# Kernel optimization log

Measured on AMD Instinct MI355X. Metric: run time of the kernel, lower is better.

The kernel has to match this reference:

```python
import jax, jax.numpy as jnp
import numpy as np

EPS = 1e-12

def setup_inputs() -> dict:
    key = jax.random.key(0)
    k1, k2 = jax.random.split(key)
    B, C, H, W = 16, 256, 64, 64
    x1 = jax.random.normal(k1, (B, C, H, W), dtype=jnp.float32)
    x2 = jax.random.normal(k2, (B, C, H, W), dtype=jnp.float32)
    return {"x1": x1, "x2": x2}

def _l2norm(x):
    # F.normalize(p=2, dim=2, eps=1e-12): divide by max(norm, eps)
    n = jnp.linalg.norm(x, axis=2, keepdims=True)
    return x / jnp.maximum(n, EPS)

def reference(x1, x2):
    B, C, H, W = x1.shape
    x111 = x1.reshape(B, C, H * W)            # [B,C,N]
    x211 = x2.reshape(B, C, H * W)
    x11 = _l2norm(x111)
    x21 = _l2norm(x211)
    # four CxC score matmuls, fused pairwise adds
    attn1 = jnp.einsum('bcn,bdn->bcd', x11, x11)
    attn2 = jnp.einsum('bcn,bdn->bcd', x21, x21)
    attn0 = jnp.einsum('bcn,bdn->bcd', x21, x11)
    attn00 = jnp.einsum('bcn,bdn->bcd', x11, x21)
    attn11 = jax.nn.softmax(attn1 + attn0, axis=-1)   # [B,C,C]
    attn22 = jax.nn.softmax(attn2 + attn00, axis=-1)
    # back-projection, torch transpose(1,2).reshape(B,C,H,W) semantics
    y1 = jnp.einsum('bcd,bdn->bcn', attn11, x111)     # [B,C,N]
    y2 = jnp.einsum('bcd,bdn->bcn', attn22, x211)
    x1_o = jnp.swapaxes(y1, 1, 2).reshape(B, C, H, W) + x1
    x2_o = jnp.swapaxes(y2, 1, 2).reshape(B, C, H, W) + x2
    return x1_o + x2_o
```

## Files before the change

### kernel.cpp

```cpp
#include <hip/hip_runtime.h>
#include <hip/hip_bf16.h>

#define B_ 16
#define C_ 256
#define N_ 4096
#define CN_ (C_ * N_)

typedef __attribute__((ext_vector_type(8))) short bf16x8_t;
typedef __attribute__((ext_vector_type(4))) float f32x4_t;

__device__ __forceinline__ unsigned short f2bf(float f) {
    __hip_bfloat16 h = __float2bfloat16(f);
    return __builtin_bit_cast(unsigned short, h);
}
__device__ __forceinline__ float bf2f(unsigned short u) {
    return __builtin_bit_cast(float, (unsigned int)u << 16);
}

__global__ __launch_bounds__(256) void knorm(const float* __restrict__ x1,
                                             const float* __restrict__ x2,
                                             unsigned short* __restrict__ x1n,
                                             unsigned short* __restrict__ x2n,
                                             float* __restrict__ norms) {
    int row = blockIdx.x;
    int t = threadIdx.x;
    const float4* r1 = (const float4*)(x1 + (size_t)row * N_);
    const float4* r2 = (const float4*)(x2 + (size_t)row * N_);
    float4 a[4], b[4];
    float s1 = 0.f, s2 = 0.f;
#pragma unroll
    for (int p = 0; p < 4; ++p) {
        a[p] = r1[p * 256 + t];
        b[p] = r2[p * 256 + t];
        s1 += a[p].x * a[p].x + a[p].y * a[p].y + a[p].z * a[p].z + a[p].w * a[p].w;
        s2 += b[p].x * b[p].x + b[p].y * b[p].y + b[p].z * b[p].z + b[p].w * b[p].w;
    }
#pragma unroll
    for (int m = 32; m; m >>= 1) { s1 += __shfl_xor(s1, m); s2 += __shfl_xor(s2, m); }
    __shared__ float red[2][4];
    int wid = t >> 6;
    if ((t & 63) == 0) { red[0][wid] = s1; red[1][wid] = s2; }
    __syncthreads();
    s1 = red[0][0] + red[0][1] + red[0][2] + red[0][3];
    s2 = red[1][0] + red[1][1] + red[1][2] + red[1][3];
    float n1 = fmaxf(sqrtf(s1), 1e-12f);
    float n2 = fmaxf(sqrtf(s2), 1e-12f);
    if (t == 0) {
        int bb = row >> 8, cc = row & 255;
        norms[(bb * 2 + 0) * 256 + cc] = n1;
        norms[(bb * 2 + 1) * 256 + cc] = n2;
    }
    float i1 = 1.0f / n1, i2 = 1.0f / n2;
    unsigned short* o1 = x1n + (size_t)row * N_;
    unsigned short* o2 = x2n + (size_t)row * N_;
#pragma unroll
    for (int p = 0; p < 4; ++p) {
        ushort4 w1, w2;
        w1.x = f2bf(a[p].x * i1); w1.y = f2bf(a[p].y * i1);
        w1.z = f2bf(a[p].z * i1); w1.w = f2bf(a[p].w * i1);
        w2.x = f2bf(b[p].x * i2); w2.y = f2bf(b[p].y * i2);
        w2.z = f2bf(b[p].z * i2); w2.w = f2bf(b[p].w * i2);
        *(ushort4*)(o1 + (size_t)(p * 256 + t) * 4) = w1;
        *(ushort4*)(o2 + (size_t)(p * 256 + t) * 4) = w2;
    }
}

__device__ __forceinline__ uint4 bf16x8_add(uint4 a, uint4 b) {
    const unsigned short* pa = (const unsigned short*)&a;
    const unsigned short* pb = (const unsigned short*)&b;
    uint4 res;
    unsigned short* pr = (unsigned short*)&res;
#pragma unroll
    for (int i = 0; i < 8; ++i) pr[i] = f2bf(bf2f(pa[i]) + bf2f(pb[i]));
    return res;
}

__global__ __launch_bounds__(256) void klogits(const unsigned short* __restrict__ x1n,
                                               const unsigned short* __restrict__ x2n,
                                               float* __restrict__ logits) {
    int bid = blockIdx.x;
    int xcd = bid & 7;
    int u = bid >> 3;
    int b = xcd + 8 * (u & 1);
    int tw = u >> 1;
    int w = tw & 1;
    int tile = tw >> 1;
    int c0 = (tile & 3) * 64;
    int d0 = (tile >> 2) * 64;

    const unsigned short* A1 = x1n + (size_t)b * CN_;
    const unsigned short* A2 = x2n + (size_t)b * CN_;
    const unsigned short* Bp = (w ? x2n : x1n) + (size_t)b * CN_;

    __shared__ unsigned short sA[64][72];
    __shared__ unsigned short sB[64][72];

    int t = threadIdx.x, lane = t & 63, wid = t >> 6;
    int wc = wid >> 1, wd = wid & 1;

    f32x4_t acc[2][2];
#pragma unroll
    for (int i = 0; i < 2; ++i)
#pragma unroll
        for (int j = 0; j < 2; ++j) acc[i][j] = 0.f;

    int srow = t >> 3, scol = (t & 7) * 8;

    for (int ks = 0; ks < 64; ++ks) {
        int k0 = ks * 64;
#pragma unroll
        for (int p = 0; p < 2; ++p) {
            int r = srow + p * 32;
            uint4 va = *(const uint4*)(A1 + (size_t)(c0 + r) * N_ + k0 + scol);
            uint4 vb = *(const uint4*)(A2 + (size_t)(c0 + r) * N_ + k0 + scol);
            *(uint4*)&sA[r][scol] = bf16x8_add(va, vb);
            uint4 vB = *(const uint4*)(Bp + (size_t)(d0 + r) * N_ + k0 + scol);
            *(uint4*)&sB[r][scol] = vB;
        }
        __syncthreads();
#pragma unroll
        for (int ksub = 0; ksub < 2; ++ksub) {
            int kc = ksub * 32 + (lane >> 4) * 8;
            bf16x8_t a0 = *(const bf16x8_t*)&sA[wc * 32 + (lane & 15)][kc];
            bf16x8_t a1 = *(const bf16x8_t*)&sA[wc * 32 + 16 + (lane & 15)][kc];
            bf16x8_t b0 = *(const bf16x8_t*)&sB[wd * 32 + (lane & 15)][kc];
            bf16x8_t b1 = *(const bf16x8_t*)&sB[wd * 32 + 16 + (lane & 15)][kc];
            acc[0][0] = __builtin_amdgcn_mfma_f32_16x16x32_bf16(a0, b0, acc[0][0], 0, 0, 0);
            acc[0][1] = __builtin_amdgcn_mfma_f32_16x16x32_bf16(a0, b1, acc[0][1], 0, 0, 0);
            acc[1][0] = __builtin_amdgcn_mfma_f32_16x16x32_bf16(a1, b0, acc[1][0], 0, 0, 0);
            acc[1][1] = __builtin_amdgcn_mfma_f32_16x16x32_bf16(a1, b1, acc[1][1], 0, 0, 0);
        }
        __syncthreads();
    }

    float* outp = logits + ((size_t)((b * 2 + w) * 256 + c0 + wc * 32)) * 256 + d0 + wd * 32;
    int orow = (lane >> 4) * 4, ocol = lane & 15;
#pragma unroll
    for (int mi = 0; mi < 2; ++mi)
#pragma unroll
        for (int ni = 0; ni < 2; ++ni)
#pragma unroll
            for (int r = 0; r < 4; ++r)
                outp[(size_t)(mi * 16 + orow + r) * 256 + ni * 16 + ocol] = acc[mi][ni][r];
}

__global__ __launch_bounds__(64) void ksoftmax(const float* __restrict__ logits,
                                               const float* __restrict__ norms,
                                               unsigned short* __restrict__ attnp) {
    int rid = blockIdx.x;
    int l = threadIdx.x;
    const float* row = logits + (size_t)rid * 256;
    int bw = rid >> 8;
    float v[4];
    float m = -1e30f;
#pragma unroll
    for (int j = 0; j < 4; ++j) { v[j] = row[j * 64 + l]; m = fmaxf(m, v[j]); }
#pragma unroll
    for (int s = 32; s; s >>= 1) m = fmaxf(m, __shfl_xor(m, s));
    float sum = 0.f;
#pragma unroll
    for (int j = 0; j < 4; ++j) { v[j] = __expf(v[j] - m); sum += v[j]; }
#pragma unroll
    for (int s = 32; s; s >>= 1) sum += __shfl_xor(sum, s);
    float rs = 1.0f / sum;
    unsigned short* outp = attnp + (size_t)rid * 256;
    const float* nr = norms + (size_t)bw * 256;
#pragma unroll
    for (int j = 0; j < 4; ++j)
        outp[j * 64 + l] = f2bf(v[j] * rs * nr[j * 64 + l]);
}

__global__ __launch_bounds__(256) void kout(const unsigned short* __restrict__ x1n,
                                            const unsigned short* __restrict__ x2n,
                                            const unsigned short* __restrict__ attnp,
                                            const float* __restrict__ x1,
                                            const float* __restrict__ x2,
                                            float* __restrict__ out) {
    int bid = blockIdx.x;
    int xcd = bid & 7;
    int u = bid >> 3;
    int b = xcd + 8 * (u & 1);
    int rest = u >> 1;
    int n0 = (rest >> 1) * 64;
    int c0 = (rest & 1) * 128;

    __shared__ unsigned short sA1[64][72];
    __shared__ unsigned short sA2[64][72];
    __shared__ unsigned short sB1[128][72];
    __shared__ unsigned short sB2[128][72];

    const unsigned short* A1 = x1n + (size_t)b * CN_;
    const unsigned short* A2 = x2n + (size_t)b * CN_;
    const unsigned short* B1 = attnp + ((size_t)(b * 2 + 0) * 256 + c0) * 256;
    const unsigned short* B2 = attnp + ((size_t)(b * 2 + 1) * 256 + c0) * 256;

    int t = threadIdx.x, lane = t & 63, wc = t >> 6;

    f32x4_t acc1[4][2], acc2[4][2];
#pragma unroll
    for (int i = 0; i < 4; ++i)
#pragma unroll
        for (int j = 0; j < 2; ++j) { acc1[i][j] = 0.f; acc2[i][j] = 0.f; }

    int dl = t >> 3, n8 = (t & 7) * 8;

    for (int ks = 0; ks < 4; ++ks) {
        int k0 = ks * 64;
#pragma unroll
        for (int p = 0; p < 2; ++p) {
            int d = dl + p * 32;
            uint4 va = *(const uint4*)(A1 + (size_t)(k0 + d) * N_ + n0 + n8);
            const unsigned short* pv = (const unsigned short*)&va;
#pragma unroll
            for (int j = 0; j < 8; ++j) sA1[n8 + j][d] = pv[j];
            uint4 vb = *(const uint4*)(A2 + (size_t)(k0 + d) * N_ + n0 + n8);
            const unsigned short* pw = (const unsigned short*)&vb;
#pragma unroll
            for (int j = 0; j < 8; ++j) sA2[n8 + j][d] = pw[j];
        }
#pragma unroll
        for (int p = 0; p < 4; ++p) {
            int cc = dl + p * 32;
            *(uint4*)&sB1[cc][n8] = *(const uint4*)(B1 + (size_t)cc * 256 + k0 + n8);
            *(uint4*)&sB2[cc][n8] = *(const uint4*)(B2 + (size_t)cc * 256 + k0 + n8);
        }
        __syncthreads();
#pragma unroll
        for (int ksub = 0; ksub < 2; ++ksub) {
            int kc = ksub * 32 + (lane >> 4) * 8;
            bf16x8_t a1f[4], a2f[4], b1f[2], b2f[2];
#pragma unroll
            for (int mi = 0; mi < 4; ++mi) {
                a1f[mi] = *(const bf16x8_t*)&sA1[mi * 16 + (lane & 15)][kc];
                a2f[mi] = *(const bf16x8_t*)&sA2[mi * 16 + (lane & 15)][kc];
            }
#pragma unroll
            for (int ci = 0; ci < 2; ++ci) {
                b1f[ci] = *(const bf16x8_t*)&sB1[wc * 32 + ci * 16 + (lane & 15)][kc];
                b2f[ci] = *(const bf16x8_t*)&sB2[wc * 32 + ci * 16 + (lane & 15)][kc];
            }
#pragma unroll
            for (int mi = 0; mi < 4; ++mi)
#pragma unroll
                for (int ci = 0; ci < 2; ++ci) {
                    acc1[mi][ci] = __builtin_amdgcn_mfma_f32_16x16x32_bf16(a1f[mi], b1f[ci], acc1[mi][ci], 0, 0, 0);
                    acc2[mi][ci] = __builtin_amdgcn_mfma_f32_16x16x32_bf16(a2f[mi], b2f[ci], acc2[mi][ci], 0, 0, 0);
                }
        }
        __syncthreads();
    }

    const size_t obase = (size_t)b * CN_;
    int orow = (lane >> 4) * 4, ocol = lane & 15;
#pragma unroll
    for (int mi = 0; mi < 4; ++mi)
#pragma unroll
        for (int ci = 0; ci < 2; ++ci)
#pragma unroll
            for (int r = 0; r < 4; ++r) {
                int n = n0 + mi * 16 + orow + r;
                int c = c0 + wc * 32 + ci * 16 + ocol;
                size_t f = obase + (size_t)n * 256 + c;
                out[f] = acc1[mi][ci][r] + acc2[mi][ci][r] + x1[f] + x2[f];
            }
}

extern "C" void kernel_launch(void* const* d_in, const int* in_sizes, int n_in,
                              void* d_out, int out_size, void* d_ws, size_t ws_size,
                              hipStream_t stream) {
    const float* x1 = (const float*)d_in[0];
    const float* x2 = (const float*)d_in[1];
    float* out = (float*)d_out;

    char* ws = (char*)d_ws;
    unsigned short* x1n  = (unsigned short*)(ws);
    unsigned short* x2n  = (unsigned short*)(ws + 33554432);
    float*          logits = (float*)(ws + 67108864);
    unsigned short* attnp  = (unsigned short*)(ws + 75497472);
    float*          norms  = (float*)(ws + 79691776);

    knorm<<<4096, 256, 0, stream>>>(x1, x2, x1n, x2n, norms);
    klogits<<<512, 256, 0, stream>>>(x1n, x2n, logits);
    ksoftmax<<<8192, 64, 0, stream>>>(logits, norms, attnp);
    kout<<<2048, 256, 0, stream>>>(x1n, x2n, attnp, x1, x2, out);
}
```

Baseline: 297.8 us.

## Precompute normalized sum and bf16 residual, use direct global-to-LDS loads with swizzle

knorm now also writes the sum of the two normalized inputs and a bf16 copy of x1+x2. This removes the per-tile bf16 add in klogits and lets kout read a bf16 residual instead of two fp32 inputs. klogits computes both logit halves in one block that shares the A tile, and stages tiles with global_load_lds into XOR-swizzled LDS. kout loads attention tiles the same way and transposes the A tile into swizzled LDS, and ksoftmax packs four rows per block. The residual rounded to bf16 loses accuracy in the output, and knorm writes more data.

Result: faster. 272.6 us (-8.5%).

```diff
diff --git a/kernel.cpp b/kernel.cpp
--- a/kernel.cpp
+++ b/kernel.cpp
@@ -8,19 +8,29 @@
 
 typedef __attribute__((ext_vector_type(8))) short bf16x8_t;
 typedef __attribute__((ext_vector_type(4))) float f32x4_t;
-
-__device__ __forceinline__ unsigned short f2bf(float f) {
+typedef unsigned int u32;
+typedef unsigned short u16;
+
+__device__ __forceinline__ u16 f2bf(float f) {
     __hip_bfloat16 h = __float2bfloat16(f);
-    return __builtin_bit_cast(unsigned short, h);
-}
-__device__ __forceinline__ float bf2f(unsigned short u) {
-    return __builtin_bit_cast(float, (unsigned int)u << 16);
+    return __builtin_bit_cast(u16, h);
+}
+__device__ __forceinline__ float bf2f(u16 u) {
+    return __builtin_bit_cast(float, (u32)u << 16);
+}
+
+__device__ __forceinline__ void gl_lds16(const void* g, void* l) {
+    __builtin_amdgcn_global_load_lds(
+        (const __attribute__((address_space(1))) u32*)(g),
+        (__attribute__((address_space(3))) u32*)(l), 16, 0, 0);
 }
 
 __global__ __launch_bounds__(256) void knorm(const float* __restrict__ x1,
                                              const float* __restrict__ x2,
-                                             unsigned short* __restrict__ x1n,
-                                             unsigned short* __restrict__ x2n,
+                                             u16* __restrict__ x1n,
+                                             u16* __restrict__ x2n,
+                                             u16* __restrict__ sN,
+                                             u16* __restrict__ sxb,
                                              float* __restrict__ norms) {
     int row = blockIdx.x;
     int t = threadIdx.x;
@@ -51,104 +61,118 @@
         norms[(bb * 2 + 1) * 256 + cc] = n2;
     }
     float i1 = 1.0f / n1, i2 = 1.0f / n2;
-    unsigned short* o1 = x1n + (size_t)row * N_;
-    unsigned short* o2 = x2n + (size_t)row * N_;
+    u16* o1 = x1n + (size_t)row * N_;
+    u16* o2 = x2n + (size_t)row * N_;
+    u16* os = sN + (size_t)row * N_;
+    u16* or_ = sxb + (size_t)row * N_;
 #pragma unroll
     for (int p = 0; p < 4; ++p) {
-        ushort4 w1, w2;
+        ushort4 w1, w2, ws, wr;
         w1.x = f2bf(a[p].x * i1); w1.y = f2bf(a[p].y * i1);
         w1.z = f2bf(a[p].z * i1); w1.w = f2bf(a[p].w * i1);
         w2.x = f2bf(b[p].x * i2); w2.y = f2bf(b[p].y * i2);
         w2.z = f2bf(b[p].z * i2); w2.w = f2bf(b[p].w * i2);
-        *(ushort4*)(o1 + (size_t)(p * 256 + t) * 4) = w1;
-        *(ushort4*)(o2 + (size_t)(p * 256 + t) * 4) = w2;
-    }
-}
-
-__device__ __forceinline__ uint4 bf16x8_add(uint4 a, uint4 b) {
-    const unsigned short* pa = (const unsigned short*)&a;
-    const unsigned short* pb = (const unsigned short*)&b;
-    uint4 res;
-    unsigned short* pr = (unsigned short*)&res;
-#pragma unroll
-    for (int i = 0; i < 8; ++i) pr[i] = f2bf(bf2f(pa[i]) + bf2f(pb[i]));
-    return res;
-}
-
-__global__ __launch_bounds__(256) void klogits(const unsigned short* __restrict__ x1n,
-                                               const unsigned short* __restrict__ x2n,
+        ws.x = f2bf(a[p].x * i1 + b[p].x * i2); ws.y = f2bf(a[p].y * i1 + b[p].y * i2);
+        ws.z = f2bf(a[p].z * i1 + b[p].z * i2); ws.w = f2bf(a[p].w * i1 + b[p].w * i2);
+        wr.x = f2bf(a[p].x + b[p].x); wr.y = f2bf(a[p].y + b[p].y);
+        wr.z = f2bf(a[p].z + b[p].z); wr.w = f2bf(a[p].w + b[p].w);
+        size_t off = (size_t)(p * 256 + t) * 4;
+        *(ushort4*)(o1 + off) = w1;
+        *(ushort4*)(o2 + off) = w2;
+        *(ushort4*)(os + off) = ws;
+        *(ushort4*)(or_ + off) = wr;
+    }
+}
+
+__global__ __launch_bounds__(256) void klogits(const u16* __restrict__ sN,
+                                               const u16* __restrict__ x1n,
+                                               const u16* __restrict__ x2n,
                                                float* __restrict__ logits) {
     int bid = blockIdx.x;
     int xcd = bid & 7;
     int u = bid >> 3;
     int b = xcd + 8 * (u & 1);
-    int tw = u >> 1;
-    int w = tw & 1;
-    int tile = tw >> 1;
+    int tile = u >> 1;
     int c0 = (tile & 3) * 64;
     int d0 = (tile >> 2) * 64;
 
-    const unsigned short* A1 = x1n + (size_t)b * CN_;
-    const unsigned short* A2 = x2n + (size_t)b * CN_;
-    const unsigned short* Bp = (w ? x2n : x1n) + (size_t)b * CN_;
-
-    __shared__ unsigned short sA[64][72];
-    __shared__ unsigned short sB[64][72];
+    __shared__ u16 lds[3 * 4096];
 
     int t = threadIdx.x, lane = t & 63, wid = t >> 6;
-    int wc = wid >> 1, wd = wid & 1;
-
-    f32x4_t acc[2][2];
+    int w = wid & 1, chalf = wid >> 1;
+
+    const char* tb[3];
+    tb[0] = (const char*)(sN  + (size_t)b * CN_ + (size_t)c0 * N_);
+    tb[1] = (const char*)(x1n + (size_t)b * CN_ + (size_t)d0 * N_);
+    tb[2] = (const char*)(x2n + (size_t)b * CN_ + (size_t)d0 * N_);
+    const char* gsrc[6];
+    char* ldst[6];
+#pragma unroll
+    for (int qq = 0; qq < 6; ++qq) {
+        int q = wid * 6 + qq;
+        int ti = q >> 3;
+        int s0 = (q & 7) * 1024 + lane * 16;
+        int rrow = s0 >> 7, inner = s0 & 127;
+        gsrc[qq] = tb[ti] + (size_t)rrow * (N_ * 2) + (inner ^ ((rrow & 7) << 4));
+        ldst[qq] = (char*)lds + q * 1024;
+    }
+
+    f32x4_t acc[2][4];
 #pragma unroll
     for (int i = 0; i < 2; ++i)
 #pragma unroll
-        for (int j = 0; j < 2; ++j) acc[i][j] = 0.f;
-
-    int srow = t >> 3, scol = (t & 7) * 8;
+        for (int j = 0; j < 4; ++j) acc[i][j] = 0.f;
+
+    const char* Abase = (const char*)lds;
+    const char* Bbase = (const char*)(lds + (1 + w) * 4096);
+    int kl = (lane >> 4) * 16;
+    int rA0 = chalf * 32 + (lane & 15);
 
     for (int ks = 0; ks < 64; ++ks) {
-        int k0 = ks * 64;
-#pragma unroll
-        for (int p = 0; p < 2; ++p) {
-            int r = srow + p * 32;
-            uint4 va = *(const uint4*)(A1 + (size_t)(c0 + r) * N_ + k0 + scol);
-            uint4 vb = *(const uint4*)(A2 + (size_t)(c0 + r) * N_ + k0 + scol);
-            *(uint4*)&sA[r][scol] = bf16x8_add(va, vb);
-            uint4 vB = *(const uint4*)(Bp + (size_t)(d0 + r) * N_ + k0 + scol);
-            *(uint4*)&sB[r][scol] = vB;
+        int kbyte = ks * 128;
+#pragma unroll
+        for (int qq = 0; qq < 6; ++qq)
+            gl_lds16(gsrc[qq] + kbyte, ldst[qq]);
+        __syncthreads();
+#pragma unroll
+        for (int ksub = 0; ksub < 2; ++ksub) {
+            int kc = ksub * 64 + kl;
+            bf16x8_t af[2], bfr[4];
+#pragma unroll
+            for (int mi = 0; mi < 2; ++mi) {
+                int rr = rA0 + mi * 16;
+                af[mi] = *(const bf16x8_t*)(Abase + ((rr << 7) + (kc ^ ((rr & 7) << 4))));
+            }
+#pragma unroll
+            for (int ni = 0; ni < 4; ++ni) {
+                int rr = ni * 16 + (lane & 15);
+                bfr[ni] = *(const bf16x8_t*)(Bbase + ((rr << 7) + (kc ^ ((rr & 7) << 4))));
+            }
+#pragma unroll
+            for (int mi = 0; mi < 2; ++mi)
+#pragma unroll
+                for (int ni = 0; ni < 4; ++ni)
+                    acc[mi][ni] = __builtin_amdgcn_mfma_f32_16x16x32_bf16(af[mi], bfr[ni], acc[mi][ni], 0, 0, 0);
         }
         __syncthreads();
-#pragma unroll
-        for (int ksub = 0; ksub < 2; ++ksub) {
-            int kc = ksub * 32 + (lane >> 4) * 8;
-            bf16x8_t a0 = *(const bf16x8_t*)&sA[wc * 32 + (lane & 15)][kc];
-            bf16x8_t a1 = *(const bf16x8_t*)&sA[wc * 32 + 16 + (lane & 15)][kc];
-            bf16x8_t b0 = *(const bf16x8_t*)&sB[wd * 32 + (lane & 15)][kc];
-            bf16x8_t b1 = *(const bf16x8_t*)&sB[wd * 32 + 16 + (lane & 15)][kc];
-            acc[0][0] = __builtin_amdgcn_mfma_f32_16x16x32_bf16(a0, b0, acc[0][0], 0, 0, 0);
-            acc[0][1] = __builtin_amdgcn_mfma_f32_16x16x32_bf16(a0, b1, acc[0][1], 0, 0, 0);
-            acc[1][0] = __builtin_amdgcn_mfma_f32_16x16x32_bf16(a1, b0, acc[1][0], 0, 0, 0);
-            acc[1][1] = __builtin_amdgcn_mfma_f32_16x16x32_bf16(a1, b1, acc[1][1], 0, 0, 0);
-        }
-        __syncthreads();
-    }
-
-    float* outp = logits + ((size_t)((b * 2 + w) * 256 + c0 + wc * 32)) * 256 + d0 + wd * 32;
+    }
+
+    float* outp = logits + ((size_t)((b * 2 + w) * 256 + c0 + chalf * 32)) * 256 + d0;
     int orow = (lane >> 4) * 4, ocol = lane & 15;
 #pragma unroll
     for (int mi = 0; mi < 2; ++mi)
 #pragma unroll
-        for (int ni = 0; ni < 2; ++ni)
+        for (int ni = 0; ni < 4; ++ni)
 #pragma unroll
             for (int r = 0; r < 4; ++r)
                 outp[(size_t)(mi * 16 + orow + r) * 256 + ni * 16 + ocol] = acc[mi][ni][r];
 }
 
-__global__ __launch_bounds__(64) void ksoftmax(const float* __restrict__ logits,
-                                               const float* __restrict__ norms,
-                                               unsigned short* __restrict__ attnp) {
-    int rid = blockIdx.x;
-    int l = threadIdx.x;
+__global__ __launch_bounds__(256) void ksoftmax(const float* __restrict__ logits,
+                                                const float* __restrict__ norms,
+                                                u16* __restrict__ attnp) {
+    int rid = blockIdx.x * 4 + (threadIdx.x >> 6);
+    int l = threadIdx.x & 63;
     const float* row = logits + (size_t)rid * 256;
     int bw = rid >> 8;
     float v[4];
@@ -163,18 +187,17 @@
 #pragma unroll
     for (int s = 32; s; s >>= 1) sum += __shfl_xor(sum, s);
     float rs = 1.0f / sum;
-    unsigned short* outp = attnp + (size_t)rid * 256;
+    u16* outp = attnp + (size_t)rid * 256;
     const float* nr = norms + (size_t)bw * 256;
 #pragma unroll
     for (int j = 0; j < 4; ++j)
         outp[j * 64 + l] = f2bf(v[j] * rs * nr[j * 64 + l]);
 }
 
-__global__ __launch_bounds__(256) void kout(const unsigned short* __restrict__ x1n,
-                                            const unsigned short* __restrict__ x2n,
-                                            const unsigned short* __restrict__ attnp,
-                                            const float* __restrict__ x1,
-                                            const float* __restrict__ x2,
+__global__ __launch_bounds__(256) void kout(const u16* __restrict__ x1n,
+                                            const u16* __restrict__ x2n,
+                                            const u16* __restrict__ attnp,
+                                            const u16* __restrict__ sxb,
                                             float* __restrict__ out) {
     int bid = blockIdx.x;
     int xcd = bid & 7;
@@ -184,17 +207,32 @@
     int n0 = (rest >> 1) * 64;
     int c0 = (rest & 1) * 128;
 
-    __shared__ unsigned short sA1[64][72];
-    __shared__ unsigned short sA2[64][72];
-    __shared__ unsigned short sB1[128][72];
-    __shared__ unsigned short sB2[128][72];
-
-    const unsigned short* A1 = x1n + (size_t)b * CN_;
-    const unsigned short* A2 = x2n + (size_t)b * CN_;
-    const unsigned short* B1 = attnp + ((size_t)(b * 2 + 0) * 256 + c0) * 256;
-    const unsigned short* B2 = attnp + ((size_t)(b * 2 + 1) * 256 + c0) * 256;
-
-    int t = threadIdx.x, lane = t & 63, wc = t >> 6;
+    __shared__ u16 sA[2][4096];
+    __shared__ u16 sB[2][8192];
+
+    int t = threadIdx.x, lane = t & 63, wid = t >> 6;
+    int wc = wid;
+
+    int tensorA = t >> 7;
+    int tt = t & 127;
+    int dq = (tt & 15) * 4;
+    int n8 = (tt >> 4) * 8;
+    const u16* Asrc = (tensorA ? x2n : x1n) + (size_t)b * CN_ + n0 + n8;
+    char* sAme = (char*)&sA[tensorA][0];
+
+    const char* gB[8];
+    char* lB[8];
+#pragma unroll
+    for (int qq = 0; qq < 8; ++qq) {
+        int q = wid * 8 + qq;
+        int tensor = q >> 4;
+        int s0 = (q & 15) * 1024 + lane * 16;
+        int rrow = s0 >> 7, inner = s0 & 127;
+        gB[qq] = (const char*)attnp +
+                 ((size_t)((b * 2 + tensor) * 256 + c0 + rrow) * 256) * 2 +
+                 (inner ^ ((rrow & 7) << 4));
+        lB[qq] = (char*)&sB[0][0] + q * 1024;
+    }
 
     f32x4_t acc1[4][2], acc2[4][2];
 #pragma unroll
@@ -202,42 +240,52 @@
 #pragma unroll
         for (int j = 0; j < 2; ++j) { acc1[i][j] = 0.f; acc2[i][j] = 0.f; }
 
-    int dl = t >> 3, n8 = (t & 7) * 8;
+    int kl = (lane >> 4) * 16;
+    const char* A0 = (const char*)&sA[0][0];
+    const char* A1 = (const char*)&sA[1][0];
+    const char* B0 = (const char*)&sB[0][0];
+    const char* B1 = (const char*)&sB[1][0];
 
     for (int ks = 0; ks < 4; ++ks) {
         int k0 = ks * 64;
 #pragma unroll
-        for (int p = 0; p < 2; ++p) {
-            int d = dl + p * 32;
-            uint4 va = *(const uint4*)(A1 + (size_t)(k0 + d) * N_ + n0 + n8);
-            const unsigned short* pv = (const unsigned short*)&va;
-#pragma unroll
-            for (int j = 0; j < 8; ++j) sA1[n8 + j][d] = pv[j];
-            uint4 vb = *(const uint4*)(A2 + (size_t)(k0 + d) * N_ + n0 + n8);
-            const unsigned short* pw = (const unsigned short*)&vb;
-#pragma unroll
-            for (int j = 0; j < 8; ++j) sA2[n8 + j][d] = pw[j];
-        }
-#pragma unroll
-        for (int p = 0; p < 4; ++p) {
-            int cc = dl + p * 32;
-            *(uint4*)&sB1[cc][n8] = *(const uint4*)(B1 + (size_t)cc * 256 + k0 + n8);
-            *(uint4*)&sB2[cc][n8] = *(const uint4*)(B2 + (size_t)cc * 256 + k0 + n8);
+        for (int qq = 0; qq < 8; ++qq)
+            gl_lds16(gB[qq] + k0 * 2, lB[qq]);
+        uint4 r0 = *(const uint4*)(Asrc + (size_t)(k0 + dq + 0) * N_);
+        uint4 r1 = *(const uint4*)(Asrc + (size_t)(k0 + dq + 1) * N_);
+        uint4 r2 = *(const uint4*)(Asrc + (size_t)(k0 + dq + 2) * N_);
+        uint4 r3 = *(const uint4*)(Asrc + (size_t)(k0 + dq + 3) * N_);
+        const u16* p0 = (const u16*)&r0;
+        const u16* p1 = (const u16*)&r1;
+        const u16* p2 = (const u16*)&r2;
+        const u16* p3 = (const u16*)&r3;
+#pragma unroll
+        for (int i = 0; i < 8; ++i) {
+            u32 lo = (u32)p0[i] | ((u32)p1[i] << 16);
+            u32 hi = (u32)p2[i] | ((u32)p3[i] << 16);
+            int n = n8 + i;
+            int addr = (n << 7) + (((dq << 1)) ^ ((n & 7) << 4));
+            uint2 val; val.x = lo; val.y = hi;
+            *(uint2*)(sAme + addr) = val;
         }
         __syncthreads();
 #pragma unroll
         for (int ksub = 0; ksub < 2; ++ksub) {
-            int kc = ksub * 32 + (lane >> 4) * 8;
+            int kc = ksub * 64 + kl;
             bf16x8_t a1f[4], a2f[4], b1f[2], b2f[2];
 #pragma unroll
             for (int mi = 0; mi < 4; ++mi) {
-                a1f[mi] = *(const bf16x8_t*)&sA1[mi * 16 + (lane & 15)][kc];
-                a2f[mi] = *(const bf16x8_t*)&sA2[mi * 16 + (lane & 15)][kc];
+                int rr = mi * 16 + (lane & 15);
+                int ao = (rr << 7) + (kc ^ ((rr & 7) << 4));
+                a1f[mi] = *(const bf16x8_t*)(A0 + ao);
+                a2f[mi] = *(const bf16x8_t*)(A1 + ao);
             }
 #pragma unroll
             for (int ci = 0; ci < 2; ++ci) {
-                b1f[ci] = *(const bf16x8_t*)&sB1[wc * 32 + ci * 16 + (lane & 15)][kc];
-                b2f[ci] = *(const bf16x8_t*)&sB2[wc * 32 + ci * 16 + (lane & 15)][kc];
+                int rr = wc * 32 + ci * 16 + (lane & 15);
+                int bo = (rr << 7) + (kc ^ ((rr & 7) << 4));
+                b1f[ci] = *(const bf16x8_t*)(B0 + bo);
+                b2f[ci] = *(const bf16x8_t*)(B1 + bo);
             }
 #pragma unroll
             for (int mi = 0; mi < 4; ++mi)
@@ -261,7 +309,7 @@
                 int n = n0 + mi * 16 + orow + r;
                 int c = c0 + wc * 32 + ci * 16 + ocol;
                 size_t f = obase + (size_t)n * 256 + c;
-                out[f] = acc1[mi][ci][r] + acc2[mi][ci][r] + x1[f] + x2[f];
+                out[f] = acc1[mi][ci][r] + acc2[mi][ci][r] + bf2f(sxb[f]);
             }
 }
 
@@ -273,14 +321,16 @@
     float* out = (float*)d_out;
 
     char* ws = (char*)d_ws;
-    unsigned short* x1n  = (unsigned short*)(ws);
-    unsigned short* x2n  = (unsigned short*)(ws + 33554432);
-    float*          logits = (float*)(ws + 67108864);
-    unsigned short* attnp  = (unsigned short*)(ws + 75497472);
-    float*          norms  = (float*)(ws + 79691776);
-
-    knorm<<<4096, 256, 0, stream>>>(x1, x2, x1n, x2n, norms);
-    klogits<<<512, 256, 0, stream>>>(x1n, x2n, logits);
-    ksoftmax<<<8192, 64, 0, stream>>>(logits, norms, attnp);
-    kout<<<2048, 256, 0, stream>>>(x1n, x2n, attnp, x1, x2, out);
-}
+    u16*   x1n    = (u16*)(ws);
+    u16*   x2n    = (u16*)(ws + 33554432ull);
+    u16*   sN     = (u16*)(ws + 67108864ull);
+    u16*   sxb    = (u16*)(ws + 100663296ull);
+    float* logits = (float*)(ws + 134217728ull);
+    u16*   attnp  = (u16*)(ws + 142606336ull);
+    float* norms  = (float*)(ws + 146800640ull);
+
+    knorm<<<4096, 256, 0, stream>>>(x1, x2, x1n, x2n, sN, sxb, norms);
+    klogits<<<256, 256, 0, stream>>>(sN, x1n, x2n, logits);
+    ksoftmax<<<2048, 256, 0, stream>>>(logits, norms, attnp);
+    kout<<<2048, 256, 0, stream>>>(x1n, x2n, attnp, sxb, out);
+}
```
